# Performance work log

Measured on AMD Instinct MI355X. Metric: run time of the kernel, lower is better.

Reference implementation:

```python
import jax, jax.numpy as jnp
import numpy as np

N = 10000   # nodes
E = 40000   # edges
D = 256     # d_model
H = 32      # num_heads
DK = 16     # d_k == d_v
L = 5       # decoder layers
SQRT_DK = float(np.sqrt(DK))


def layer_norm(x, g, b, eps=1e-5):
    m = x.mean(-1, keepdims=True)
    v = ((x - m) ** 2).mean(-1, keepdims=True)
    return (x - m) / jnp.sqrt(v + eps) * g + b


def mha(x, edge_index, We, Wq, Wk, Wv, Wo, bo):
    # x: [N, D]
    xe = x @ We.T                                   # embed, no bias
    Q = (xe @ Wq.T).reshape(N, H, DK)               # [N, H, dk]
    K = (xe @ Wk.T).reshape(N, H, DK)
    V = (xe @ Wv.T).reshape(N, H, DK)
    src, dst = edge_index[0], edge_index[1]          # message j->i, aggregate at dst
    Qi = Q[dst]                                      # [E, H, dk]
    Kj = K[src]
    Vj = V[src]
    # torch split_heads gives [*, dk, H]; Q_i @ K_j^T contracts over the HEAD axis
    alpha = jnp.einsum('eha,ehb->eab', Qi, Kj) / SQRT_DK   # [E, dk, dk]
    att = jax.nn.softmax(alpha, axis=-1)                    # per-edge softmax over last dk axis
    msg = jnp.einsum('eab,ehb->eah', att, Vj)               # [E, dk, H]
    agg = jax.ops.segment_sum(msg, dst, num_segments=N)     # [N, dk, H] scatter-add
    attn_out = jnp.transpose(agg, (0, 2, 1)).reshape(N, H * DK)  # combine_heads
    # dropout is identity at inference
    return xe + attn_out @ Wo.T + bo


def decoder(edge_index, x, We, Wq, Wk, Wv, Wo, bo, ln_g, ln_b, mlp_W, mlp_b):
    for l in range(L):
        h = mha(x, edge_index, We[l, 0], Wq[l, 0], Wk[l, 0], Wv[l, 0], Wo[l, 0], bo[l, 0])
        x = layer_norm(x + h, ln_g[l, 0], ln_b[l, 0])
        h = mha(x, edge_index, We[l, 1], Wq[l, 1], Wk[l, 1], Wv[l, 1], Wo[l, 1], bo[l, 1])
        x = layer_norm(x + h, ln_g[l, 1], ln_b[l, 1])
        x = layer_norm(x + x @ mlp_W[l].T + mlp_b[l], ln_g[l, 2], ln_b[l, 2])
    return x


def setup_inputs() -> dict:
    key = jax.random.key(0)
    ks = jax.random.split(key, 10)
    s = 0.05
    return {
        'edge_index': jax.random.randint(ks[0], (2, E), 0, N, dtype=jnp.int32),
        'x': jax.random.normal(ks[1], (N, D), dtype=jnp.float32),
        'We': jax.random.normal(ks[2], (L, 2, D, D), dtype=jnp.float32) * s,
        'Wq': jax.random.normal(ks[3], (L, 2, H * DK, D), dtype=jnp.float32) * s,
        'Wk': jax.random.normal(ks[4], (L, 2, H * DK, D), dtype=jnp.float32) * s,
        'Wv': jax.random.normal(ks[5], (L, 2, H * DK, D), dtype=jnp.float32) * s,
        'Wo': jax.random.normal(ks[6], (L, 2, D, H * DK), dtype=jnp.float32) * s,
        'bo': jnp.zeros((L, 2, D), dtype=jnp.float32),
        'ln_g': jnp.ones((L, 3, D), dtype=jnp.float32),
        'ln_b': jnp.zeros((L, 3, D), dtype=jnp.float32),
        'mlp_W': jax.random.normal(ks[7], (L, D, D), dtype=jnp.float32) * s,
        'mlp_b': jnp.zeros((L, D), dtype=jnp.float32),
    }


def reference(edge_index, x, We, Wq, Wk, Wv, Wo, bo, ln_g, ln_b, mlp_W, mlp_b):
    return decoder(edge_index, x, We, Wq, Wk, Wv, Wo, bo, ln_g, ln_b, mlp_W, mlp_b)
```

## Files before the change

### kernel.cpp

```cpp
#include <hip/hip_runtime.h>
#include <hip/hip_bf16.h>

#define N_NODES 10000
#define N_EDGES 40000
#define NLAYERS 5

typedef __bf16 bf16x8 __attribute__((ext_vector_type(8)));
typedef __bf16 bf16x4 __attribute__((ext_vector_type(4)));
typedef float  f32x4  __attribute__((ext_vector_type(4)));

__device__ __forceinline__ bf16x8 cvt8(float4 a, float4 b) {
    bf16x8 r;
    r[0] = (__bf16)a.x; r[1] = (__bf16)a.y; r[2] = (__bf16)a.z; r[3] = (__bf16)a.w;
    r[4] = (__bf16)b.x; r[5] = (__bf16)b.y; r[6] = (__bf16)b.z; r[7] = (__bf16)b.w;
    return r;
}

__device__ __forceinline__ void gload_lds16(const void* g, void* l) {
    __builtin_amdgcn_global_load_lds(
        (const __attribute__((address_space(1))) void*)g,
        (__attribute__((address_space(3))) void*)l, 16, 0, 0);
}

__global__ __launch_bounds__(256) void prep_cvt(
    const float* __restrict__ We, const float* __restrict__ Wq,
    const float* __restrict__ Wk, const float* __restrict__ Wv,
    const float* __restrict__ Wo, const float* __restrict__ mlpW,
    const float* __restrict__ x_in,
    __bf16* __restrict__ wMerged, __bf16* __restrict__ wQKVtmp,
    __bf16* __restrict__ wOd, __bf16* __restrict__ wMd, __bf16* __restrict__ xbb)
{
    const int reg = blockIdx.y;
    long i0 = (long)blockIdx.x * blockDim.x + threadIdx.x;
    long stride = (long)gridDim.x * blockDim.x;
    if (reg == 0) {
        for (long i = i0; i < 81920; i += stride) {
            long e = i * 8; long ch = e >> 16; long r = e & 65535;
            *(bf16x8*)(wMerged + ch * 458752 + r) =
                cvt8(*(const float4*)(We + e), *(const float4*)(We + e + 4));
        }
    } else if (reg == 1 || reg == 2) {
        const float* S = (reg == 1) ? Wq : Wk;
        __bf16* D = wQKVtmp + ((reg == 2) ? 131072 : 0);
        for (long i = i0; i < 163840; i += stride) {
            long e = i * 8;
            int slot = (int)(e >> 17); int rem = (int)(e & 131071);
            int row = rem >> 8; int col = rem & 255;
            int srow = ((row & 31) << 4) | (row >> 5);
            const float* sp = S + ((long)slot << 17) + ((long)srow << 8) + col;
            *(bf16x8*)(D + (long)slot * 393216 + ((long)row << 8) + col) =
                cvt8(*(const float4*)sp, *(const float4*)(sp + 4));
        }
    } else if (reg == 3) {
        for (long i = i0; i < 163840; i += stride) {
            long e = i * 8; long ch = e >> 17; long r = e & 131071;
            *(bf16x8*)(wQKVtmp + 262144 + ch * 393216 + r) =
                cvt8(*(const float4*)(Wv + e), *(const float4*)(Wv + e + 4));
        }
    } else if (reg == 4) {
        for (long i = i0; i < 163840; i += stride) {
            long e = i * 8;
            *(bf16x8*)(wOd + e) =
                cvt8(*(const float4*)(Wo + e), *(const float4*)(Wo + e + 4));
        }
    } else if (reg == 5) {
        for (long i = i0; i < 40960; i += stride) {
            long e = i * 8;
            *(bf16x8*)(wMd + e) =
                cvt8(*(const float4*)(mlpW + e), *(const float4*)(mlpW + e + 4));
        }
    } else {
        for (long i = i0; i < 320000; i += stride) {
            long e = i * 8;
            *(bf16x8*)(xbb + e) =
                cvt8(*(const float4*)(x_in + e), *(const float4*)(x_in + e + 4));
        }
    }
}

__global__ __launch_bounds__(256) void transpose_we(
    const float* __restrict__ S, __bf16* __restrict__ D)
{
    __shared__ float tile[64][65];
    const int slot = blockIdx.y;
    const int tx = blockIdx.x & 3, ty = blockIdx.x >> 2;
    const float* sp = S + (size_t)slot * 65536 + (size_t)(ty * 64) * 256 + tx * 64;
    const int t = threadIdx.x;
    #pragma unroll
    for (int j = 0; j < 16; ++j) {
        int idx = t + 256 * j;
        int r = idx >> 6, c = idx & 63;
        tile[r][c] = sp[r * 256 + c];
    }
    __syncthreads();
    __bf16* dp = D + (size_t)slot * 65536 + (size_t)(tx * 64) * 256 + ty * 64;
    #pragma unroll
    for (int j = 0; j < 16; ++j) {
        int idx = t + 256 * j;
        int nl = idx >> 6, kl = idx & 63;
        dp[nl * 256 + kl] = (__bf16)tile[kl][nl];
    }
}

__global__ __launch_bounds__(256) void hist_dst(
    const int* __restrict__ eidx, int* __restrict__ counts)
{
    int e = blockIdx.x * 256 + threadIdx.x;
    if (e < N_EDGES) atomicAdd(&counts[eidx[N_EDGES + e]], 1);
}

__global__ __launch_bounds__(256) void scan_offsets(
    const int* __restrict__ counts, int* __restrict__ offs,
    int* __restrict__ wrk, int n)
{
    const int tid = threadIdx.x;
    const int base = tid * 40;
    int local[40];
    int s = 0;
    #pragma unroll
    for (int j = 0; j < 40; ++j) {
        int i = base + j;
        int v = (i < n) ? counts[i] : 0;
        local[j] = s; s += v;
    }
    __shared__ int sm[256];
    sm[tid] = s;
    __syncthreads();
    for (int off = 1; off < 256; off <<= 1) {
        int t2 = (tid >= off) ? sm[tid - off] : 0;
        __syncthreads();
        sm[tid] += t2;
        __syncthreads();
    }
    int pre = (tid == 0) ? 0 : sm[tid - 1];
    #pragma unroll
    for (int j = 0; j < 40; ++j) {
        int i = base + j;
        if (i < n) { int v = pre + local[j]; offs[i] = v; wrk[i] = v; }
    }
    if (tid == 255) offs[n] = sm[255];
}

__global__ __launch_bounds__(256) void scatter_csr(
    const int* __restrict__ eidx, int* __restrict__ wrk, int* __restrict__ csr_src)
{
    int e = blockIdx.x * 256 + threadIdx.x;
    if (e < N_EDGES) {
        int sn = eidx[e];
        int d  = eidx[N_EDGES + e];
        int pos = atomicAdd(&wrk[d], 1);
        csr_src[pos] = sn;
    }
}

template<int MODE, int BN>
__global__ __launch_bounds__(256) void gemm_lds(
    const __bf16* __restrict__ A, const __bf16* __restrict__ W,
    float* __restrict__ Cf, __bf16* __restrict__ Ch,
    int M, int K, int ldc, long sA, long sW, long sC)
{
    __shared__ __bf16 As[128 * 64];
    __shared__ __bf16 Wsh[BN * 64];
    constexpr int NF = BN / 32;
    A += (long)blockIdx.z * sA;
    W += (long)blockIdx.z * sW;
    if (Ch) Ch += (long)blockIdx.z * sC;
    const int tid = threadIdx.x;
    const int ln  = tid & 63;
    const int wv  = tid >> 6;
    const int wr  = wv >> 1, wc = wv & 1;
    const int brow0 = blockIdx.y * 128;
    const int colb0 = blockIdx.x * BN;

    const int srow = ln >> 3;
    const int scol = ((ln & 7) ^ srow) * 8;
    const int fr = ln & 15;
    const int kq = ln >> 4;
    char* asb = (char*)As;
    char* wsb = (char*)Wsh;

    f32x4 acc[4][NF];
    #pragma unroll
    for (int m = 0; m < 4; ++m)
        #pragma unroll
        for (int n = 0; n < NF; ++n) acc[m][n] = (f32x4){0.f, 0.f, 0.f, 0.f};

    const int nt = K >> 6;
    for (int t = 0; t < nt; ++t) {
        const int kk0 = t << 6;
        if (t) __syncthreads();
        #pragma unroll
        for (int c = 0; c < 4; ++c) {
            int ch = wv * 4 + c;
            int grow = brow0 + ch * 8 + srow;
            if (grow >= M) grow = M - 1;
            gload_lds16(A + (size_t)grow * K + kk0 + scol, asb + ch * 1024);
        }
        #pragma unroll
        for (int c = 0; c < NF; ++c) {
            int ch = wv * NF + c;
            int grow = colb0 + ch * 8 + srow;
            gload_lds16(W + (size_t)grow * K + kk0 + scol, wsb + ch * 1024);
        }
        __syncthreads();
        #pragma unroll
        for (int ks = 0; ks < 2; ++ks) {
            const int kb = ks * 64 + kq * 16;
            const int sw = (fr & 7) << 4;
            bf16x8 af[4], wf[NF];
            #pragma unroll
            for (int m = 0; m < 4; ++m) {
                int row = wr * 64 + m * 16 + fr;
                af[m] = *(const bf16x8*)(asb + row * 128 + (kb ^ sw));
            }
            #pragma unroll
            for (int n = 0; n < NF; ++n) {
                int row = wc * (BN / 2) + n * 16 + fr;
                wf[n] = *(const bf16x8*)(wsb + row * 128 + (kb ^ sw));
            }
            #pragma unroll
            for (int m = 0; m < 4; ++m)
                #pragma unroll
                for (int n = 0; n < NF; ++n)
                    acc[m][n] = __builtin_amdgcn_mfma_f32_16x16x32_bf16(
                        af[m], wf[n], acc[m][n], 0, 0, 0);
        }
    }

    const int rq = (ln >> 4) * 4;
    #pragma unroll
    for (int m = 0; m < 4; ++m) {
        #pragma unroll
        for (int rr = 0; rr < 4; ++rr) {
            int orow = brow0 + wr * 64 + m * 16 + rq + rr;
            if (orow < M) {
                #pragma unroll
                for (int n = 0; n < NF; ++n) {
                    int c = colb0 + wc * (BN / 2) + fr + n * 16;
                    if (MODE == 0)      Cf[(size_t)orow * ldc + c] = acc[m][n][rr];
                    else if (MODE == 1) Ch[(size_t)orow * ldc + c] = (__bf16)acc[m][n][rr];
                    else {
                        if (c < 256) Ch[(size_t)orow * 256 + c] = (__bf16)acc[m][n][rr];
                        else ((__bf16*)Cf)[(size_t)orow * 1536 + (c - 256)] = (__bf16)acc[m][n][rr];
                    }
                }
            }
        }
    }
}

__global__ __launch_bounds__(256) void edge_attn_csr(
    const int* __restrict__ csr_off, const int* __restrict__ csr_src,
    const __bf16* __restrict__ qkv, __bf16* __restrict__ attn_bf)
{
    const int lane = threadIdx.x & 63;
    const int d = blockIdx.x * 4 + (threadIdx.x >> 6);
    const int fr = lane & 15;
    const int G  = lane >> 4;

    const __bf16* qT = qkv + (size_t)d * 1536;
    const bf16x8 qf = *(const bf16x8*)(qT + fr * 32 + G * 8);

    const f32x4 zero = {0.f, 0.f, 0.f, 0.f};
    f32x4 acc0 = zero, acc1 = zero;

    const int i0 = csr_off[d], i1 = csr_off[d + 1];
    int sN = (i0 < i1) ? csr_src[i0] : 0;
    bf16x8 kfN = *(const bf16x8*)(qkv + (size_t)sN * 1536 + 512 + fr * 32 + G * 8);
    for (int i = i0; i < i1; ++i) {
        const int s = sN;
        const bf16x8 kf = kfN;
        if (i + 1 < i1) {
            sN = csr_src[i + 1];
            kfN = *(const bf16x8*)(qkv + (size_t)sN * 1536 + 512 + fr * 32 + G * 8);
        }
        const __bf16* vp = qkv + (size_t)s * 1536 + 1024;
        bf16x8 vf0 = {0, 0, 0, 0, 0, 0, 0, 0};
        bf16x8 vf1 = {0, 0, 0, 0, 0, 0, 0, 0};
        if (G < 2) {
            vf0 = *(const bf16x8*)(vp + fr * 16 + G * 8);
            vf1 = *(const bf16x8*)(vp + (16 + fr) * 16 + G * 8);
        }
        f32x4 al = __builtin_amdgcn_mfma_f32_16x16x32_bf16(kf, qf, zero, 0, 0, 0);

        float mx = fmaxf(fmaxf(al[0], al[1]), fmaxf(al[2], al[3]));
        mx = fmaxf(mx, __shfl_xor(mx, 16));
        mx = fmaxf(mx, __shfl_xor(mx, 32));
        float p[4];
        #pragma unroll
        for (int r = 0; r < 4; ++r) p[r] = __expf((al[r] - mx) * 0.25f);
        float sum = p[0] + p[1] + p[2] + p[3];
        sum += __shfl_xor(sum, 16);
        sum += __shfl_xor(sum, 32);
        const float inv = 1.f / sum;

        bf16x8 paf;
        #pragma unroll
        for (int j = 0; j < 8; ++j) {
            int srcLane = fr + ((G * 8 + j) >> 2) * 16;
            float v = __shfl(p[j & 3], srcLane);
            paf[j] = (G < 2) ? (__bf16)(v * inv) : (__bf16)0.f;
        }

        acc0 = __builtin_amdgcn_mfma_f32_16x16x32_bf16(paf, vf0, acc0, 0, 0, 0);
        acc1 = __builtin_amdgcn_mfma_f32_16x16x32_bf16(paf, vf1, acc1, 0, 0, 0);
    }

    __bf16* ob = attn_bf + (size_t)d * 512;
    bf16x4 o0, o1;
    #pragma unroll
    for (int r = 0; r < 4; ++r) { o0[r] = (__bf16)acc0[r]; o1[r] = (__bf16)acc1[r]; }
    *(bf16x4*)(ob + fr * 16 + G * 4)       = o0;
    *(bf16x4*)(ob + 256 + fr * 16 + G * 4) = o1;
}

template<bool CHAIN>
__global__ __launch_bounds__(256) void fused_tail(
    const __bf16* __restrict__ A, const __bf16* __restrict__ W,
    const __bf16* __restrict__ xres, const __bf16* __restrict__ tb,
    const float* __restrict__ bias, const float* __restrict__ g1,
    const float* __restrict__ b1,
    const __bf16* __restrict__ Wm, const float* __restrict__ mb,
    const float* __restrict__ g2, const float* __restrict__ b2,
    float* __restrict__ outf, __bf16* __restrict__ outb, int M)
{
    __shared__ __bf16 As[32 * 64];
    __shared__ __bf16 Wsh[256 * 64];
    __shared__ __bf16 X1[CHAIN ? 32 * 256 : 2];
    __shared__ float sm_s[4][32];
    __shared__ float sm_q[4][32];
    const int tid = threadIdx.x;
    const int ln  = tid & 63;
    const int wv  = tid >> 6;
    const int fr  = ln & 15;
    const int kq  = ln >> 4;
    const int brow0 = blockIdx.x * 32;
    const int srow = ln >> 3;
    const int scol = ((ln & 7) ^ srow) * 8;
    char* asb = (char*)As;
    char* wsb = (char*)Wsh;
    char* x1b = (char*)X1;
    const f32x4 zero = {0.f, 0.f, 0.f, 0.f};

    f32x4 acc[2][4];
    #pragma unroll
    for (int m = 0; m < 2; ++m)
        #pragma unroll
        for (int n = 0; n < 4; ++n) acc[m][n] = zero;

    for (int t = 0; t < 8; ++t) {
        const int kk0 = t << 6;
        if (t) __syncthreads();
        {
            int grow = brow0 + wv * 8 + srow;
            if (grow >= M) grow = M - 1;
            gload_lds16(A + (size_t)grow * 512 + kk0 + scol, asb + wv * 1024);
        }
        #pragma unroll
        for (int c = 0; c < 8; ++c) {
            int ch = wv * 8 + c;
            gload_lds16(W + (size_t)(ch * 8 + srow) * 512 + kk0 + scol, wsb + ch * 1024);
        }
        __syncthreads();
        #pragma unroll
        for (int ks = 0; ks < 2; ++ks) {
            const int kb = ks * 64 + kq * 16;
            const int sw = (fr & 7) << 4;
            bf16x8 af0 = *(const bf16x8*)(asb + fr * 128 + (kb ^ sw));
            bf16x8 af1 = *(const bf16x8*)(asb + (16 + fr) * 128 + (kb ^ sw));
            #pragma unroll
            for (int n = 0; n < 4; ++n) {
                bf16x8 wf = *(const bf16x8*)(wsb + (wv * 64 + n * 16 + fr) * 128 + (kb ^ sw));
                acc[0][n] = __builtin_amdgcn_mfma_f32_16x16x32_bf16(af0, wf, acc[0][n], 0, 0, 0);
                acc[1][n] = __builtin_amdgcn_mfma_f32_16x16x32_bf16(af1, wf, acc[1][n], 0, 0, 0);
            }
        }
    }

    float s2[2][4], q2[2][4];
    #pragma unroll
    for (int m = 0; m < 2; ++m)
        #pragma unroll
        for (int rr = 0; rr < 4; ++rr) { s2[m][rr] = 0.f; q2[m][rr] = 0.f; }
    #pragma unroll
    for (int m = 0; m < 2; ++m)
        #pragma unroll
        for (int n = 0; n < 4; ++n) {
            const int col = wv * 64 + n * 16 + fr;
            const float bi = bias[col];
            #pragma unroll
            for (int rr = 0; rr < 4; ++rr) {
                int gr = brow0 + m * 16 + kq * 4 + rr; if (gr >= M) gr = M - 1;
                float v = acc[m][n][rr] + (float)xres[(size_t)gr * 256 + col]
                          + (float)tb[(size_t)gr * 256 + col] + bi;
                acc[m][n][rr] = v;
                s2[m][rr] += v; q2[m][rr] += v * v;
            }
        }
    #pragma unroll
    for (int mask = 1; mask < 16; mask <<= 1)
        #pragma unroll
        for (int m = 0; m < 2; ++m)
            #pragma unroll
            for (int rr = 0; rr < 4; ++rr) {
                s2[m][rr] += __shfl_xor(s2[m][rr], mask);
                q2[m][rr] += __shfl_xor(q2[m][rr], mask);
            }
    if (fr == 0) {
        #pragma unroll
        for (int m = 0; m < 2; ++m)
            #pragma unroll
            for (int rr = 0; rr < 4; ++rr) {
                sm_s[wv][m * 16 + kq * 4 + rr] = s2[m][rr];
                sm_q[wv][m * 16 + kq * 4 + rr] = q2[m][rr];
            }
    }
    __syncthreads();
    float mean[2][4], invs[2][4];
    #pragma unroll
    for (int m = 0; m < 2; ++m)
        #pragma unroll
        for (int rr = 0; rr < 4; ++rr) {
            int rw = m * 16 + kq * 4 + rr;
            float ts = sm_s[0][rw] + sm_s[1][rw] + sm_s[2][rw] + sm_s[3][rw];
            float tq = sm_q[0][rw] + sm_q[1][rw] + sm_q[2][rw] + sm_q[3][rw];
            float mn = ts * (1.f / 256.f);
            mean[m][rr] = mn;
            invs[m][rr] = rsqrtf(tq * (1.f / 256.f) - mn * mn + 1e-5f);
        }

    if (!CHAIN) {
        #pragma unroll
        for (int m = 0; m < 2; ++m)
            #pragma unroll
            for (int n = 0; n < 4; ++n) {
                const int col = wv * 64 + n * 16 + fr;
                const float gv = g1[col], bv = b1[col];
                #pragma unroll
                for (int rr = 0; rr < 4; ++rr) {
                    int gr = brow0 + m * 16 + kq * 4 + rr;
                    if (gr < M) {
                        float o = (acc[m][n][rr] - mean[m][rr]) * invs[m][rr] * gv + bv;
                        outb[(size_t)gr * 256 + col] = (__bf16)o;
                        if (outf) outf[(size_t)gr * 256 + col] = o;
                    }
                }
            }
        return;
    }

    #pragma unroll
    for (int m = 0; m < 2; ++m)
        #pragma unroll
        for (int n = 0; n < 4; ++n) {
            const int col = wv * 64 + n * 16 + fr;
            const float gv = g1[col], bv = b1[col];
            #pragma unroll
            for (int rr = 0; rr < 4; ++rr) {
                int row = m * 16 + kq * 4 + rr;
                float o = (acc[m][n][rr] - mean[m][rr]) * invs[m][rr] * gv + bv;
                *(__bf16*)(x1b + row * 512 + ((col * 2) ^ ((row & 7) << 4))) = (__bf16)o;
            }
        }
    __syncthreads();

    f32x4 acc2[2][4];
    #pragma unroll
    for (int m = 0; m < 2; ++m)
        #pragma unroll
        for (int n = 0; n < 4; ++n) acc2[m][n] = zero;

    for (int t = 0; t < 4; ++t) {
        if (t) __syncthreads();
        #pragma unroll
        for (int c = 0; c < 8; ++c) {
            int ch = wv * 8 + c;
            gload_lds16(Wm + (size_t)(ch * 8 + srow) * 256 + t * 64 + scol, wsb + ch * 1024);
        }
        __syncthreads();
        #pragma unroll
        for (int ks = 0; ks < 2; ++ks) {
            const int kb = t * 128 + ks * 64 + kq * 16;
            const int sw = (fr & 7) << 4;
            bf16x8 af0 = *(const bf16x8*)(x1b + fr * 512 + (kb ^ sw));
            bf16x8 af1 = *(const bf16x8*)(x1b + (16 + fr) * 512 + (kb ^ ((fr & 7) << 4)));
            const int kbl = ks * 64 + kq * 16;
            #pragma unroll
            for (int n = 0; n < 4; ++n) {
                bf16x8 wf = *(const bf16x8*)(wsb + (wv * 64 + n * 16 + fr) * 128 + (kbl ^ sw));
                acc2[0][n] = __builtin_amdgcn_mfma_f32_16x16x32_bf16(af0, wf, acc2[0][n], 0, 0, 0);
                acc2[1][n] = __builtin_amdgcn_mfma_f32_16x16x32_bf16(af1, wf, acc2[1][n], 0, 0, 0);
            }
        }
    }

    #pragma unroll
    for (int m = 0; m < 2; ++m)
        #pragma unroll
        for (int rr = 0; rr < 4; ++rr) { s2[m][rr] = 0.f; q2[m][rr] = 0.f; }
    #pragma unroll
    for (int m = 0; m < 2; ++m)
        #pragma unroll
        for (int n = 0; n < 4; ++n) {
            const int col = wv * 64 + n * 16 + fr;
            const float bi = mb[col];
            #pragma unroll
            for (int rr = 0; rr < 4; ++rr) {
                int row = m * 16 + kq * 4 + rr;
                float x1v = (float)*(const __bf16*)(x1b + row * 512 + ((col * 2) ^ ((row & 7) << 4)));
                float v = acc2[m][n][rr] + x1v + bi;
                acc2[m][n][rr] = v;
                s2[m][rr] += v; q2[m][rr] += v * v;
            }
        }
    #pragma unroll
    for (int mask = 1; mask < 16; mask <<= 1)
        #pragma unroll
        for (int m = 0; m < 2; ++m)
            #pragma unroll
            for (int rr = 0; rr < 4; ++rr) {
                s2[m][rr] += __shfl_xor(s2[m][rr], mask);
                q2[m][rr] += __shfl_xor(q2[m][rr], mask);
            }
    __syncthreads();
    if (fr == 0) {
        #pragma unroll
        for (int m = 0; m < 2; ++m)
            #pragma unroll
            for (int rr = 0; rr < 4; ++rr) {
                sm_s[wv][m * 16 + kq * 4 + rr] = s2[m][rr];
                sm_q[wv][m * 16 + kq * 4 + rr] = q2[m][rr];
            }
    }
    __syncthreads();
    #pragma unroll
    for (int m = 0; m < 2; ++m)
        #pragma unroll
        for (int rr = 0; rr < 4; ++rr) {
            int rw = m * 16 + kq * 4 + rr;
            float ts = sm_s[0][rw] + sm_s[1][rw] + sm_s[2][rw] + sm_s[3][rw];
            float tq = sm_q[0][rw] + sm_q[1][rw] + sm_q[2][rw] + sm_q[3][rw];
            float mn = ts * (1.f / 256.f);
            mean[m][rr] = mn;
            invs[m][rr] = rsqrtf(tq * (1.f / 256.f) - mn * mn + 1e-5f);
        }
    #pragma unroll
    for (int m = 0; m < 2; ++m)
        #pragma unroll
        for (int n = 0; n < 4; ++n) {
            const int col = wv * 64 + n * 16 + fr;
            const float gv = g2[col], bv = b2[col];
            #pragma unroll
            for (int rr = 0; rr < 4; ++rr) {
                int gr = brow0 + m * 16 + kq * 4 + rr;
                if (gr < M) {
                    float o = (acc2[m][n][rr] - mean[m][rr]) * invs[m][rr] * gv + bv;
                    outb[(size_t)gr * 256 + col] = (__bf16)o;
                    if (outf) outf[(size_t)gr * 256 + col] = o;
                }
            }
        }
}

extern "C" void kernel_launch(void* const* d_in, const int* in_sizes, int n_in,
                              void* d_out, int out_size, void* d_ws, size_t ws_size,
                              hipStream_t stream)
{
    const int*   eidx = (const int*)  d_in[0];
    const float* x_in = (const float*)d_in[1];
    const float* We   = (const float*)d_in[2];
    const float* Wq   = (const float*)d_in[3];
    const float* Wk   = (const float*)d_in[4];
    const float* Wv   = (const float*)d_in[5];
    const float* Wo   = (const float*)d_in[6];
    const float* bo   = (const float*)d_in[7];
    const float* lng  = (const float*)d_in[8];
    const float* lnb  = (const float*)d_in[9];
    const float* mlpW = (const float*)d_in[10];
    const float* mlpb = (const float*)d_in[11];
    float* out = (float*)d_out;

    char* p = (char*)d_ws;
    __bf16* wMerged = (__bf16*)p; p += (size_t)10 * 458752 * 2;
    __bf16* wQKVtmp = (__bf16*)p; p += (size_t)10 * 393216 * 2;
    __bf16* wET     = (__bf16*)p; p += (size_t)10 * 65536  * 2;
    __bf16* wO      = (__bf16*)p; p += (size_t)10 * 131072 * 2;
    __bf16* wM      = (__bf16*)p; p += (size_t)5  * 65536  * 2;
    __bf16* qkv     = (__bf16*)p; p += (size_t)N_NODES * 1536 * 2;
    __bf16* attn_bf = (__bf16*)p; p += (size_t)N_NODES * 512 * 2;
    __bf16* xeb     = (__bf16*)p; p += (size_t)N_NODES * 256 * 2;
    __bf16* xbb     = (__bf16*)p; p += (size_t)N_NODES * 256 * 2;
    int* counts  = (int*)p;    p += (size_t)(N_NODES + 16) * 4;
    int* csr_off = (int*)p;    p += (size_t)(N_NODES + 16) * 4;
    int* csr_wrk = (int*)p;    p += (size_t)(N_NODES + 16) * 4;
    int* csr_src = (int*)p;    p += (size_t)N_EDGES * 4;
    if ((size_t)(p - (char*)d_ws) > ws_size) return;

    dim3 blk(256);

    hipMemsetAsync(counts, 0, (size_t)(N_NODES + 16) * 4, stream);
    hist_dst<<<dim3(157), blk, 0, stream>>>(eidx, counts);
    scan_offsets<<<dim3(1), blk, 0, stream>>>(counts, csr_off, csr_wrk, N_NODES);
    scatter_csr<<<dim3(157), blk, 0, stream>>>(eidx, csr_wrk, csr_src);

    prep_cvt<<<dim3(128, 7), blk, 0, stream>>>(We, Wq, Wk, Wv, Wo, mlpW, x_in,
                                               wMerged, wQKVtmp, wO, wM, xbb);
    transpose_we<<<dim3(16, 10), blk, 0, stream>>>(We, wET);

    gemm_lds<1, 64><<<dim3(4, 12, 10), blk, 0, stream>>>(
        wQKVtmp, wET, nullptr, wMerged + 65536, 1536, 256, 256,
        393216, 65536, 458752);

    dim3 gMerged(14, 79);

    for (int l = 0; l < NLAYERS; ++l) {
        for (int s = 0; s < 2; ++s) {
            size_t ls = (size_t)(l * 2 + s);
            gemm_lds<3, 128><<<gMerged, blk, 0, stream>>>(
                xbb, wMerged + ls * 458752, (float*)qkv, xeb, N_NODES, 256, 0, 0, 0, 0);
            edge_attn_csr<<<dim3(N_NODES / 4), blk, 0, stream>>>(csr_off, csr_src,
                                                                 qkv, attn_bf);
            if (s == 0) {
                fused_tail<false><<<dim3(313), blk, 0, stream>>>(
                    attn_bf, wO + ls * 131072, xbb, xeb, bo + ls * 256,
                    lng + (size_t)(l * 3) * 256, lnb + (size_t)(l * 3) * 256,
                    nullptr, nullptr, nullptr, nullptr,
                    nullptr, xbb, N_NODES);
            } else {
                bool lastL = (l == NLAYERS - 1);
                fused_tail<true><<<dim3(313), blk, 0, stream>>>(
                    attn_bf, wO + ls * 131072, xbb, xeb, bo + ls * 256,
                    lng + (size_t)(l * 3 + 1) * 256, lnb + (size_t)(l * 3 + 1) * 256,
                    wM + (size_t)l * 65536, mlpb + (size_t)l * 256,
                    lng + (size_t)(l * 3 + 2) * 256, lnb + (size_t)(l * 3 + 2) * 256,
                    lastL ? out : nullptr, xbb, N_NODES);
            }
        }
    }
}
```

Before: 690.2 us.

## Restructure fused_tail GEMMs: 512 threads, full A tile in LDS, direct weight loads

The fused output-projection/LayerNorm/MLP tail kernel now runs 8 waves per block, each owning 32 output columns instead of 64. The whole 32x512 activation tile is staged into swizzled LDS once, and weight fragments are read straight from global memory instead of being staged through LDS in K-chunks. This removes the per-chunk barriers and LDS staging of weights, and gives more waves to hide latency. In exchange every block re-reads the weights from global or L2 with no LDS reuse, and the LayerNorm reductions now sum partials across 8 waves.

```diff
diff --git a/kernel.cpp b/kernel.cpp
--- a/kernel.cpp
+++ b/kernel.cpp
@@ -315,7 +315,7 @@
 }
 
 template<bool CHAIN>
-__global__ __launch_bounds__(256) void fused_tail(
+__global__ __launch_bounds__(512) void fused_tail(
     const __bf16* __restrict__ A, const __bf16* __restrict__ W,
     const __bf16* __restrict__ xres, const __bf16* __restrict__ tb,
     const float* __restrict__ bias, const float* __restrict__ g1,
@@ -324,57 +324,48 @@
     const float* __restrict__ g2, const float* __restrict__ b2,
     float* __restrict__ outf, __bf16* __restrict__ outb, int M)
 {
-    __shared__ __bf16 As[32 * 64];
-    __shared__ __bf16 Wsh[256 * 64];
+    __shared__ __bf16 As[32 * 512];
     __shared__ __bf16 X1[CHAIN ? 32 * 256 : 2];
-    __shared__ float sm_s[4][32];
-    __shared__ float sm_q[4][32];
+    __shared__ float sm_s[8][32];
+    __shared__ float sm_q[8][32];
     const int tid = threadIdx.x;
     const int ln  = tid & 63;
     const int wv  = tid >> 6;
     const int fr  = ln & 15;
     const int kq  = ln >> 4;
     const int brow0 = blockIdx.x * 32;
-    const int srow = ln >> 3;
-    const int scol = ((ln & 7) ^ srow) * 8;
     char* asb = (char*)As;
-    char* wsb = (char*)Wsh;
     char* x1b = (char*)X1;
     const f32x4 zero = {0.f, 0.f, 0.f, 0.f};
-
-    f32x4 acc[2][4];
-    #pragma unroll
-    for (int m = 0; m < 2; ++m)
-        #pragma unroll
-        for (int n = 0; n < 4; ++n) acc[m][n] = zero;
-
-    for (int t = 0; t < 8; ++t) {
-        const int kk0 = t << 6;
-        if (t) __syncthreads();
-        {
-            int grow = brow0 + wv * 8 + srow;
-            if (grow >= M) grow = M - 1;
-            gload_lds16(A + (size_t)grow * 512 + kk0 + scol, asb + wv * 1024);
-        }
-        #pragma unroll
-        for (int c = 0; c < 8; ++c) {
-            int ch = wv * 8 + c;
-            gload_lds16(W + (size_t)(ch * 8 + srow) * 512 + kk0 + scol, wsb + ch * 1024);
-        }
-        __syncthreads();
-        #pragma unroll
-        for (int ks = 0; ks < 2; ++ks) {
-            const int kb = ks * 64 + kq * 16;
-            const int sw = (fr & 7) << 4;
-            bf16x8 af0 = *(const bf16x8*)(asb + fr * 128 + (kb ^ sw));
-            bf16x8 af1 = *(const bf16x8*)(asb + (16 + fr) * 128 + (kb ^ sw));
-            #pragma unroll
-            for (int n = 0; n < 4; ++n) {
-                bf16x8 wf = *(const bf16x8*)(wsb + (wv * 64 + n * 16 + fr) * 128 + (kb ^ sw));
-                acc[0][n] = __builtin_amdgcn_mfma_f32_16x16x32_bf16(af0, wf, acc[0][n], 0, 0, 0);
-                acc[1][n] = __builtin_amdgcn_mfma_f32_16x16x32_bf16(af1, wf, acc[1][n], 0, 0, 0);
-            }
-        }
+    const int sw = (fr & 7) << 4;
+    const int colw = wv * 32;
+
+    #pragma unroll
+    for (int c = 0; c < 4; ++c) {
+        int r = wv * 4 + c;
+        int grow = brow0 + r; if (grow >= M) grow = M - 1;
+        int srcb = (ln * 16) ^ ((r & 7) << 4);
+        gload_lds16((const char*)A + (size_t)grow * 1024 + srcb, asb + r * 1024);
+    }
+    __syncthreads();
+
+    f32x4 acc[2][2];
+    #pragma unroll
+    for (int m = 0; m < 2; ++m)
+        #pragma unroll
+        for (int n = 0; n < 2; ++n) acc[m][n] = zero;
+    #pragma unroll
+    for (int kk = 0; kk < 512; kk += 32) {
+        const int kb = (kk + kq * 8) * 2;
+        bf16x8 af0 = *(const bf16x8*)(asb + fr * 1024 + (kb ^ sw));
+        bf16x8 af1 = *(const bf16x8*)(asb + (16 + fr) * 1024 + (kb ^ sw));
+        const __bf16* wp = W + (size_t)(colw + fr) * 512 + kk + kq * 8;
+        bf16x8 wf0 = *(const bf16x8*)wp;
+        bf16x8 wf1 = *(const bf16x8*)(wp + 16 * 512);
+        acc[0][0] = __builtin_amdgcn_mfma_f32_16x16x32_bf16(af0, wf0, acc[0][0], 0, 0, 0);
+        acc[1][0] = __builtin_amdgcn_mfma_f32_16x16x32_bf16(af1, wf0, acc[1][0], 0, 0, 0);
+        acc[0][1] = __builtin_amdgcn_mfma_f32_16x16x32_bf16(af0, wf1, acc[0][1], 0, 0, 0);
+        acc[1][1] = __builtin_amdgcn_mfma_f32_16x16x32_bf16(af1, wf1, acc[1][1], 0, 0, 0);
     }
 
     float s2[2][4], q2[2][4];
@@ -385,8 +376,8 @@
     #pragma unroll
     for (int m = 0; m < 2; ++m)
         #pragma unroll
-        for (int n = 0; n < 4; ++n) {
-            const int col = wv * 64 + n * 16 + fr;
+        for (int n = 0; n < 2; ++n) {
+            const int col = colw + n * 16 + fr;
             const float bi = bias[col];
             #pragma unroll
             for (int rr = 0; rr < 4; ++rr) {
@@ -422,8 +413,9 @@
         #pragma unroll
         for (int rr = 0; rr < 4; ++rr) {
             int rw = m * 16 + kq * 4 + rr;
-            float ts = sm_s[0][rw] + sm_s[1][rw] + sm_s[2][rw] + sm_s[3][rw];
-            float tq = sm_q[0][rw] + sm_q[1][rw] + sm_q[2][rw] + sm_q[3][rw];
+            float ts = 0.f, tq = 0.f;
+            #pragma unroll
+            for (int w = 0; w < 8; ++w) { ts += sm_s[w][rw]; tq += sm_q[w][rw]; }
             float mn = ts * (1.f / 256.f);
             mean[m][rr] = mn;
             invs[m][rr] = rsqrtf(tq * (1.f / 256.f) - mn * mn + 1e-5f);
@@ -433,8 +425,8 @@
         #pragma unroll
         for (int m = 0; m < 2; ++m)
             #pragma unroll
-            for (int n = 0; n < 4; ++n) {
-                const int col = wv * 64 + n * 16 + fr;
+            for (int n = 0; n < 2; ++n) {
+                const int col = colw + n * 16 + fr;
                 const float gv = g1[col], bv = b1[col];
                 #pragma unroll
                 for (int rr = 0; rr < 4; ++rr) {
@@ -452,8 +444,8 @@
     #pragma unroll
     for (int m = 0; m < 2; ++m)
         #pragma unroll
-        for (int n = 0; n < 4; ++n) {
-            const int col = wv * 64 + n * 16 + fr;
+        for (int n = 0; n < 2; ++n) {
+            const int col = colw + n * 16 + fr;
             const float gv = g1[col], bv = b1[col];
             #pragma unroll
             for (int rr = 0; rr < 4; ++rr) {
@@ -464,34 +456,23 @@
         }
     __syncthreads();
 
-    f32x4 acc2[2][4];
-    #pragma unroll
-    for (int m = 0; m < 2; ++m)
-        #pragma unroll
-        for (int n = 0; n < 4; ++n) acc2[m][n] = zero;
-
-    for (int t = 0; t < 4; ++t) {
-        if (t) __syncthreads();
-        #pragma unroll
-        for (int c = 0; c < 8; ++c) {
-            int ch = wv * 8 + c;
-            gload_lds16(Wm + (size_t)(ch * 8 + srow) * 256 + t * 64 + scol, wsb + ch * 1024);
-        }
-        __syncthreads();
-        #pragma unroll
-        for (int ks = 0; ks < 2; ++ks) {
-            const int kb = t * 128 + ks * 64 + kq * 16;
-            const int sw = (fr & 7) << 4;
-            bf16x8 af0 = *(const bf16x8*)(x1b + fr * 512 + (kb ^ sw));
-            bf16x8 af1 = *(const bf16x8*)(x1b + (16 + fr) * 512 + (kb ^ ((fr & 7) << 4)));
-            const int kbl = ks * 64 + kq * 16;
-            #pragma unroll
-            for (int n = 0; n < 4; ++n) {
-                bf16x8 wf = *(const bf16x8*)(wsb + (wv * 64 + n * 16 + fr) * 128 + (kbl ^ sw));
-                acc2[0][n] = __builtin_amdgcn_mfma_f32_16x16x32_bf16(af0, wf, acc2[0][n], 0, 0, 0);
-                acc2[1][n] = __builtin_amdgcn_mfma_f32_16x16x32_bf16(af1, wf, acc2[1][n], 0, 0, 0);
-            }
-        }
+    f32x4 acc2[2][2];
+    #pragma unroll
+    for (int m = 0; m < 2; ++m)
+        #pragma unroll
+        for (int n = 0; n < 2; ++n) acc2[m][n] = zero;
+    #pragma unroll
+    for (int kk = 0; kk < 256; kk += 32) {
+        const int kb = (kk + kq * 8) * 2;
+        bf16x8 af0 = *(const bf16x8*)(x1b + fr * 512 + (kb ^ sw));
+        bf16x8 af1 = *(const bf16x8*)(x1b + (16 + fr) * 512 + (kb ^ sw));
+        const __bf16* wp = Wm + (size_t)(colw + fr) * 256 + kk + kq * 8;
+        bf16x8 wf0 = *(const bf16x8*)wp;
+        bf16x8 wf1 = *(const bf16x8*)(wp + 16 * 256);
+        acc2[0][0] = __builtin_amdgcn_mfma_f32_16x16x32_bf16(af0, wf0, acc2[0][0], 0, 0, 0);
+        acc2[1][0] = __builtin_amdgcn_mfma_f32_16x16x32_bf16(af1, wf0, acc2[1][0], 0, 0, 0);
+        acc2[0][1] = __builtin_amdgcn_mfma_f32_16x16x32_bf16(af0, wf1, acc2[0][1], 0, 0, 0);
+        acc2[1][1] = __builtin_amdgcn_mfma_f32_16x16x32_bf16(af1, wf1, acc2[1][1], 0, 0, 0);
     }
 
     #pragma unroll
@@ -501,8 +482,8 @@
     #pragma unroll
     for (int m = 0; m < 2; ++m)
         #pragma unroll
-        for (int n = 0; n < 4; ++n) {
-            const int col = wv * 64 + n * 16 + fr;
+        for (int n = 0; n < 2; ++n) {
+            const int col = colw + n * 16 + fr;
             const float bi = mb[col];
             #pragma unroll
             for (int rr = 0; rr < 4; ++rr) {
@@ -522,7 +503,6 @@
                 s2[m][rr] += __shfl_xor(s2[m][rr], mask);
                 q2[m][rr] += __shfl_xor(q2[m][rr], mask);
             }
-    __syncthreads();
     if (fr == 0) {
         #pragma unroll
         for (int m = 0; m < 2; ++m)
@@ -538,8 +518,9 @@
         #pragma unroll
         for (int rr = 0; rr < 4; ++rr) {
             int rw = m * 16 + kq * 4 + rr;
-            float ts = sm_s[0][rw] + sm_s[1][rw] + sm_s[2][rw] + sm_s[3][rw];
-            float tq = sm_q[0][rw] + sm_q[1][rw] + sm_q[2][rw] + sm_q[3][rw];
+            float ts = 0.f, tq = 0.f;
+            #pragma unroll
+            for (int w = 0; w < 8; ++w) { ts += sm_s[w][rw]; tq += sm_q[w][rw]; }
             float mn = ts * (1.f / 256.f);
             mean[m][rr] = mn;
             invs[m][rr] = rsqrtf(tq * (1.f / 256.f) - mn * mn + 1e-5f);
@@ -547,8 +528,8 @@
     #pragma unroll
     for (int m = 0; m < 2; ++m)
         #pragma unroll
-        for (int n = 0; n < 4; ++n) {
-            const int col = wv * 64 + n * 16 + fr;
+        for (int n = 0; n < 2; ++n) {
+            const int col = colw + n * 16 + fr;
             const float gv = g2[col], bv = b2[col];
             #pragma unroll
             for (int rr = 0; rr < 4; ++rr) {
@@ -621,14 +602,14 @@
             edge_attn_csr<<<dim3(N_NODES / 4), blk, 0, stream>>>(csr_off, csr_src,
                                                                  qkv, attn_bf);
             if (s == 0) {
-                fused_tail<false><<<dim3(313), blk, 0, stream>>>(
+                fused_tail<false><<<dim3(313), dim3(512), 0, stream>>>(
                     attn_bf, wO + ls * 131072, xbb, xeb, bo + ls * 256,
                     lng + (size_t)(l * 3) * 256, lnb + (size_t)(l * 3) * 256,
                     nullptr, nullptr, nullptr, nullptr,
                     nullptr, xbb, N_NODES);
             } else {
                 bool lastL = (l == NLAYERS - 1);
-                fused_tail<true><<<dim3(313), blk, 0, stream>>>(
+                fused_tail<true><<<dim3(313), dim3(512), 0, stream>>>(
                     attn_bf, wO + ls * 131072, xbb, xeb, bo + ls * 256,
                     lng + (size_t)(l * 3 + 1) * 256, lnb + (size_t)(l * 3 + 1) * 256,
                     wM + (size_t)l * 65536, mlpb + (size_t)l * 256,
```

Result: slower. 835.0 us (+21.0%).
